# Performance work log

Hardware: AMD Instinct MI355X
Metric: run time of the kernel (lower is better)

Reference implementation:

```python
import jax, jax.numpy as jnp
import numpy as np

B, C = 16, 1024
EPS = 1e-12
TINY = 1e-9


def setup_inputs() -> dict:
    key = jax.random.key(0)
    k1, k2 = jax.random.split(key)
    lower = jax.random.normal(k1, (B, C), dtype=jnp.float32)
    # guarantee upper >= lower as required by bound propagation
    upper = lower + jax.random.uniform(k2, (B, C), dtype=jnp.float32)
    return {"lower": lower, "upper": upper}


def reference(lower, upper):
    l, u = lower, upper
    Bv, Cv = l.shape
    eye = jnp.eye(Cv, dtype=l.dtype)          # (C,C)
    offdiag = 1.0 - eye                        # zero on diagonal

    # pairwise logit differences d_ij = x_j - x_i, bounded by [l_d, u_d]; diag forced to 0
    l_d = (l[:, None, :] - u[:, :, None]) * offdiag   # (B,C,C)
    u_d = (u[:, None, :] - l[:, :, None]) * offdiag   # (B,C,C)

    exp_l = jnp.exp(l_d)
    exp_u = jnp.exp(u_d)

    # exp upper bound: secant over [l_d, u_d]
    denom = u_d - l_d
    a_u = (exp_u - exp_l) / (denom + EPS)
    a_u = jnp.where(jnp.abs(denom) < TINY, exp_u, a_u)
    b_u = exp_l - a_u * l_d

    # exp lower bound: tangent at midpoint t
    t = 0.5 * (l_d + u_d)
    a_l = jnp.exp(t)
    b_l = a_l - a_l * t                        # exp(t) - a_l * t

    # zero diagonal entries (i == j term excluded from the sum)
    a_u = a_u * offdiag
    b_u = b_u * offdiag
    a_l = a_l * offdiag
    b_l = b_l * offdiag
    exp_l_od = exp_l * offdiag
    exp_u_od = exp_u * offdiag

    S_l = exp_l_od.sum(axis=2)                 # (B,C)
    S_u = exp_u_od.sum(axis=2)                 # (B,C)

    # linear coefficients of S_i w.r.t. logits x: off-diag from a, diag collects -sum_j a_ij
    sum_a_u = a_u.sum(axis=2)                  # (B,C)
    sum_a_l = a_l.sum(axis=2)
    coef_S_upper = a_u - eye[None, :, :] * sum_a_u[:, :, None]
    coef_S_lower = a_l - eye[None, :, :] * sum_a_l[:, :, None]
    bias_S_upper = b_u.sum(axis=2)
    bias_S_lower = b_l.sum(axis=2)

    # g(S) = 1 / (1 + S), decreasing & convex
    g_at_S_l = 1.0 / (1.0 + S_l)
    g_at_S_u = 1.0 / (1.0 + S_u)

    # upper relaxation of g: tangent (secant of decreasing convex fn swaps roles)
    denom_g = S_u - S_l
    m_u = (g_at_S_u - g_at_S_l) / (denom_g + EPS)
    m_u = jnp.where(jnp.abs(denom_g) < TINY, -1.0 / (1.0 + S_u) ** 2, m_u)
    c_u = g_at_S_l - m_u * S_l

    # lower relaxation of g: tangent at S_u
    m_l = -1.0 / (1.0 + S_u) ** 2
    c_l = 1.0 / (1.0 + S_u) - m_l * S_u

    # compose (m_u >= ... careful with sign handled as in original: direct product)
    final_upper_coef = m_u[:, :, None] * coef_S_upper   # (B,C,C)
    final_lower_coef = m_l[:, :, None] * coef_S_lower   # (B,C,C)
    final_upper_bias = m_u * bias_S_upper + c_u          # (B,C)
    final_lower_bias = m_l * bias_S_lower + c_l          # (B,C)

    soft_lower = jnp.clip(g_at_S_u, 0.0, 1.0)
    soft_upper = jnp.clip(g_at_S_l, 0.0, 1.0)

    return (soft_lower, soft_upper,
            final_lower_coef, final_upper_coef,
            final_lower_bias, final_upper_bias)
```

## Files before the change

### kernel.cpp

```cpp
#include <hip/hip_runtime.h>

namespace {

constexpr int B = 16;
constexpr int C = 1024;
constexpr int BC = B * C;
constexpr long long BCC = (long long)B * C * C;
constexpr float EPS  = 1e-12f;
constexpr float TINY = 1e-9f;

__global__ __launch_bounds__(256) void bounded_softmax_kernel(
    const float* __restrict__ lower,
    const float* __restrict__ upper,
    float* __restrict__ out)
{
    const int row = blockIdx.x;
    const int b   = row >> 10;
    const int i   = row & (C - 1);
    const int tid = threadIdx.x;

    const float* __restrict__ lrow = lower + b * C;
    const float* __restrict__ urow = upper + b * C;

    const float l_i = lrow[i];
    const float u_i = urow[i];

    const float4 lj4 = *reinterpret_cast<const float4*>(lrow + tid * 4);
    const float4 uj4 = *reinterpret_cast<const float4*>(urow + tid * 4);
    const float ljv[4] = {lj4.x, lj4.y, lj4.z, lj4.w};
    const float ujv[4] = {uj4.x, uj4.y, uj4.z, uj4.w};

    float a_u[4], a_l[4];
    float acc[6] = {0.f, 0.f, 0.f, 0.f, 0.f, 0.f};

    #pragma unroll
    for (int k = 0; k < 4; ++k) {
        const int j = tid * 4 + k;
        const float l_d = ljv[k] - u_i;
        const float u_d = ujv[k] - l_i;
        const float el  = __expf(l_d);
        const float eu  = __expf(u_d);
        const float denom = u_d - l_d;
        float au = (eu - el) / (denom + EPS);
        au = (fabsf(denom) < TINY) ? eu : au;
        const float bu = fmaf(-au, l_d, el);
        const float t  = 0.5f * (l_d + u_d);
        const float al = __expf(t);
        const float bl = al * (1.0f - t);

        float elz = el, euz = eu, auz = au, buz = bu, alz = al, blz = bl;
        if (j == i) { elz = euz = auz = buz = alz = blz = 0.0f; }

        acc[0] += elz; acc[1] += euz; acc[2] += auz;
        acc[3] += alz; acc[4] += buz; acc[5] += blz;
        a_u[k] = auz; a_l[k] = alz;
    }

    __shared__ float red[4][6];
    const int lane = tid & 63;
    const int wid  = tid >> 6;
    #pragma unroll
    for (int m = 0; m < 6; ++m) {
        float v = acc[m];
        #pragma unroll
        for (int o = 32; o > 0; o >>= 1) v += __shfl_down(v, o);
        if (lane == 0) red[wid][m] = v;
    }
    __syncthreads();

    const float S_l  = red[0][0] + red[1][0] + red[2][0] + red[3][0];
    const float S_u  = red[0][1] + red[1][1] + red[2][1] + red[3][1];
    const float SA_u = red[0][2] + red[1][2] + red[2][2] + red[3][2];
    const float SA_l = red[0][3] + red[1][3] + red[2][3] + red[3][3];
    const float SB_u = red[0][4] + red[1][4] + red[2][4] + red[3][4];
    const float SB_l = red[0][5] + red[1][5] + red[2][5] + red[3][5];

    const float g_l = 1.0f / (1.0f + S_l);
    const float g_u = 1.0f / (1.0f + S_u);
    const float dg  = S_u - S_l;
    float m_u = (g_u - g_l) / (dg + EPS);
    m_u = (fabsf(dg) < TINY) ? (-g_u * g_u) : m_u;
    const float c_u = g_l - m_u * S_l;
    const float m_l = -g_u * g_u;
    const float c_l = g_u - m_l * S_u;

    float* __restrict__ lower_coef = out + 2 * BC + (long long)row * C;
    float* __restrict__ upper_coef = out + 2 * BC + BCC + (long long)row * C;

    float lv[4], uv[4];
    #pragma unroll
    for (int k = 0; k < 4; ++k) {
        const int j = tid * 4 + k;
        const float dl = (j == i) ? SA_l : 0.0f;
        const float du = (j == i) ? SA_u : 0.0f;
        lv[k] = m_l * (a_l[k] - dl);
        uv[k] = m_u * (a_u[k] - du);
    }
    *reinterpret_cast<float4*>(lower_coef + tid * 4) =
        make_float4(lv[0], lv[1], lv[2], lv[3]);
    *reinterpret_cast<float4*>(upper_coef + tid * 4) =
        make_float4(uv[0], uv[1], uv[2], uv[3]);

    if (tid == 0) {
        const float soft_lower = fminf(fmaxf(g_u, 0.0f), 1.0f);
        const float soft_upper = fminf(fmaxf(g_l, 0.0f), 1.0f);
        out[row]                          = soft_lower;
        out[BC + row]                     = soft_upper;
        out[2 * BC + 2 * BCC + row]       = fmaf(m_l, SB_l, c_l);
        out[2 * BC + 2 * BCC + BC + row]  = fmaf(m_u, SB_u, c_u);
    }
}

}

extern "C" void kernel_launch(void* const* d_in, const int* in_sizes, int n_in,
                              void* d_out, int out_size, void* d_ws, size_t ws_size,
                              hipStream_t stream) {
    const float* lower = (const float*)d_in[0];
    const float* upper = (const float*)d_in[1];
    float* out = (float*)d_out;
    bounded_softmax_kernel<<<dim3(B * C), dim3(256), 0, stream>>>(lower, upper, out);
}
```

Measured before the change: 149.9 us.

## Factor exponentials into per-element tables and split into three kernels

```diff
diff --git a/kernel.cpp b/kernel.cpp
--- a/kernel.cpp
+++ b/kernel.cpp
@@ -9,105 +9,191 @@
 constexpr float EPS  = 1e-12f;
 constexpr float TINY = 1e-9f;
 
-__global__ __launch_bounds__(256) void bounded_softmax_kernel(
-    const float* __restrict__ lower,
-    const float* __restrict__ upper,
-    float* __restrict__ out)
+typedef float vfloat4 __attribute__((ext_vector_type(4)));
+
+__global__ __launch_bounds__(256) void k0_tables(
+    const float* __restrict__ lower, const float* __restrict__ upper,
+    float* __restrict__ El, float* __restrict__ Eu,
+    float* __restrict__ Em, float* __restrict__ W,
+    float* __restrict__ Bsum)
+{
+    const int b   = blockIdx.x;
+    const int tid = threadIdx.x;
+    const int base = b * C + tid * 4;
+
+    const vfloat4 l4 = *reinterpret_cast<const vfloat4*>(lower + base);
+    const vfloat4 u4 = *reinterpret_cast<const vfloat4*>(upper + base);
+
+    vfloat4 el, eu, em, w;
+    float s0 = 0.f, s1 = 0.f, s2 = 0.f, s3 = 0.f;
+    #pragma unroll
+    for (int k = 0; k < 4; ++k) {
+        const float e_l = __expf(l4[k]);
+        const float e_u = __expf(u4[k]);
+        const float h   = 0.5f * (l4[k] + u4[k]);
+        const float e_m = __expf(h);
+        el[k] = e_l; eu[k] = e_u; em[k] = e_m; w[k] = u4[k] - l4[k];
+        s0 += e_l; s1 += e_u; s2 += e_m; s3 += e_m * (1.0f - h);
+    }
+    *reinterpret_cast<vfloat4*>(El + base) = el;
+    *reinterpret_cast<vfloat4*>(Eu + base) = eu;
+    *reinterpret_cast<vfloat4*>(Em + base) = em;
+    *reinterpret_cast<vfloat4*>(W  + base) = w;
+
+    __shared__ float red[4][4];
+    const int lane = tid & 63, wid = tid >> 6;
+    float v[4] = {s0, s1, s2, s3};
+    #pragma unroll
+    for (int m = 0; m < 4; ++m) {
+        #pragma unroll
+        for (int o = 32; o > 0; o >>= 1) v[m] += __shfl_down(v[m], o);
+        if (lane == 0) red[wid][m] = v[m];
+    }
+    __syncthreads();
+    if (tid == 0) {
+        #pragma unroll
+        for (int m = 0; m < 4; ++m)
+            Bsum[b * 4 + m] = red[0][m] + red[1][m] + red[2][m] + red[3][m];
+    }
+}
+
+__global__ __launch_bounds__(256) void k1_rows(
+    const float* __restrict__ lower, const float* __restrict__ upper,
+    const float* __restrict__ El, const float* __restrict__ Eu,
+    const float* __restrict__ Em, const float* __restrict__ W,
+    const float* __restrict__ Bsum,
+    float* __restrict__ RS, float* __restrict__ out)
 {
     const int row = blockIdx.x;
     const int b   = row >> 10;
-    const int i   = row & (C - 1);
     const int tid = threadIdx.x;
 
-    const float* __restrict__ lrow = lower + b * C;
-    const float* __restrict__ urow = upper + b * C;
-
-    const float l_i = lrow[i];
-    const float u_i = urow[i];
-
-    const float4 lj4 = *reinterpret_cast<const float4*>(lrow + tid * 4);
-    const float4 uj4 = *reinterpret_cast<const float4*>(urow + tid * 4);
-    const float ljv[4] = {lj4.x, lj4.y, lj4.z, lj4.w};
-    const float ujv[4] = {uj4.x, uj4.y, uj4.z, uj4.w};
-
-    float a_u[4], a_l[4];
-    float acc[6] = {0.f, 0.f, 0.f, 0.f, 0.f, 0.f};
-
+    const float l_i  = lower[row], u_i = upper[row];
+    const float El_i = El[row], Eu_i = Eu[row], Em_i = Em[row], w_i = W[row];
+    const float su = __builtin_amdgcn_rcpf(Eu_i);
+    const float sl = __builtin_amdgcn_rcpf(El_i);
+    const float sm = __builtin_amdgcn_rcpf(Em_i);
+
+    const int base = b * C + tid * 4;
+    const vfloat4 El4 = *reinterpret_cast<const vfloat4*>(El + base);
+    const vfloat4 Eu4 = *reinterpret_cast<const vfloat4*>(Eu + base);
+    const vfloat4 W4  = *reinterpret_cast<const vfloat4*>(W  + base);
+    const vfloat4 l4  = *reinterpret_cast<const vfloat4*>(lower + base);
+
+    float accA = 0.f, accT = 0.f;
     #pragma unroll
     for (int k = 0; k < 4; ++k) {
-        const int j = tid * 4 + k;
-        const float l_d = ljv[k] - u_i;
-        const float u_d = ujv[k] - l_i;
-        const float el  = __expf(l_d);
-        const float eu  = __expf(u_d);
-        const float denom = u_d - l_d;
-        float au = (eu - el) / (denom + EPS);
-        au = (fabsf(denom) < TINY) ? eu : au;
-        const float bu = fmaf(-au, l_d, el);
-        const float t  = 0.5f * (l_d + u_d);
-        const float al = __expf(t);
-        const float bl = al * (1.0f - t);
-
-        float elz = el, euz = eu, auz = au, buz = bu, alz = al, blz = bl;
-        if (j == i) { elz = euz = auz = buz = alz = blz = 0.0f; }
-
-        acc[0] += elz; acc[1] += euz; acc[2] += auz;
-        acc[3] += alz; acc[4] += buz; acc[5] += blz;
-        a_u[k] = auz; a_l[k] = alz;
-    }
-
-    __shared__ float red[4][6];
-    const int lane = tid & 63;
-    const int wid  = tid >> 6;
-    #pragma unroll
-    for (int m = 0; m < 6; ++m) {
-        float v = acc[m];
+        const float eu = Eu4[k] * sl;
+        const float el = El4[k] * su;
+        const float denom = W4[k] + w_i;
+        const float r = __builtin_amdgcn_rcpf(denom + EPS);
+        float a = (eu - el) * r;
+        a = (fabsf(denom) < TINY) ? eu : a;
+        accA += a;
+        accT += a * l4[k];
+    }
+
+    __shared__ float red[4][2];
+    const int lane = tid & 63, wid = tid >> 6;
+    #pragma unroll
+    for (int o = 32; o > 0; o >>= 1) accA += __shfl_down(accA, o);
+    #pragma unroll
+    for (int o = 32; o > 0; o >>= 1) accT += __shfl_down(accT, o);
+    if (lane == 0) { red[wid][0] = accA; red[wid][1] = accT; }
+    __syncthreads();
+
+    if (tid == 0) {
+        const float A_all = red[0][0] + red[1][0] + red[2][0] + red[3][0];
+        const float T_all = red[0][1] + red[1][1] + red[2][1] + red[3][1];
+
+        const float eu_d = Eu_i * sl;
+        const float el_d = El_i * su;
+        const float den_d = w_i + w_i;
+        const float r_d = __builtin_amdgcn_rcpf(den_d + EPS);
+        float a_d = (eu_d - el_d) * r_d;
+        a_d = (fabsf(den_d) < TINY) ? eu_d : a_d;
+        const float SA_u = A_all - a_d;
+        const float Tn   = T_all - a_d * l_i;
+
+        const float SEl = Bsum[b * 4 + 0];
+        const float SEu = Bsum[b * 4 + 1];
+        const float P0  = Bsum[b * 4 + 2];
+        const float P1  = Bsum[b * 4 + 3];
+
+        const float S_l  = su * (SEl - El_i);
+        const float S_u  = sl * (SEu - Eu_i);
+        const float SA_l = sm * (P0  - Em_i);
+        const float h_i  = 0.5f * (l_i + u_i);
+        const float SB_l = sm * fmaf(h_i, P0, P1) - 1.0f;
+        const float SB_u = S_l - Tn + u_i * SA_u;
+
+        const float g_l = 1.0f / (1.0f + S_l);
+        const float g_u = 1.0f / (1.0f + S_u);
+        const float dg  = S_u - S_l;
+        float m_u = (g_u - g_l) / (dg + EPS);
+        m_u = (fabsf(dg) < TINY) ? (-g_u * g_u) : m_u;
+        const float c_u = g_l - m_u * S_l;
+        const float m_l = -g_u * g_u;
+        const float c_l = g_u - m_l * S_u;
+
+        out[row]                         = fminf(fmaxf(g_u, 0.0f), 1.0f);
+        out[BC + row]                    = fminf(fmaxf(g_l, 0.0f), 1.0f);
+        out[2 * BC + 2 * BCC + row]      = fmaf(m_l, SB_l, c_l);
+        out[2 * BC + 2 * BCC + BC + row] = fmaf(m_u, SB_u, c_u);
+
+        vfloat4 rs0, rs1;
+        rs0[0] = m_u;  rs0[1] = su;        rs0[2] = sl;         rs0[3] = w_i;
+        rs1[0] = -m_u * SA_u;  rs1[1] = m_l * sm;  rs1[2] = -m_l * SA_l;  rs1[3] = 0.f;
+        *reinterpret_cast<vfloat4*>(RS + (long long)row * 8)     = rs0;
+        *reinterpret_cast<vfloat4*>(RS + (long long)row * 8 + 4) = rs1;
+    }
+}
+
+__global__ __launch_bounds__(256) void k2_stream(
+    const float* __restrict__ El, const float* __restrict__ Eu,
+    const float* __restrict__ Em, const float* __restrict__ W,
+    const float* __restrict__ RS, float* __restrict__ out)
+{
+    const int blk = blockIdx.x;
+    const int b   = blk >> 8;
+    const int ig  = blk & 255;
+    const int tid = threadIdx.x;
+    const int j0  = tid * 4;
+    const int tbase = b * C + j0;
+
+    const vfloat4 El4 = *reinterpret_cast<const vfloat4*>(El + tbase);
+    const vfloat4 Eu4 = *reinterpret_cast<const vfloat4*>(Eu + tbase);
+    const vfloat4 Em4 = *reinterpret_cast<const vfloat4*>(Em + tbase);
+    const vfloat4 W4  = *reinterpret_cast<const vfloat4*>(W  + tbase);
+
+    float* __restrict__ lower_base = out + 2 * BC;
+    float* __restrict__ upper_base = out + 2 * BC + BCC;
+
+    #pragma unroll
+    for (int r = 0; r < 4; ++r) {
+        const int i   = ig * 4 + r;
+        const int row = b * C + i;
+        const vfloat4 rs0 = *reinterpret_cast<const vfloat4*>(RS + (long long)row * 8);
+        const vfloat4 rs1 = *reinterpret_cast<const vfloat4*>(RS + (long long)row * 8 + 4);
+        const float m_u = rs0[0], su = rs0[1], sl = rs0[2], w_i = rs0[3];
+        const float DiagU = rs1[0], MlE = rs1[1], DiagL = rs1[2];
+
+        vfloat4 up, lo;
         #pragma unroll
-        for (int o = 32; o > 0; o >>= 1) v += __shfl_down(v, o);
-        if (lane == 0) red[wid][m] = v;
-    }
-    __syncthreads();
-
-    const float S_l  = red[0][0] + red[1][0] + red[2][0] + red[3][0];
-    const float S_u  = red[0][1] + red[1][1] + red[2][1] + red[3][1];
-    const float SA_u = red[0][2] + red[1][2] + red[2][2] + red[3][2];
-    const float SA_l = red[0][3] + red[1][3] + red[2][3] + red[3][3];
-    const float SB_u = red[0][4] + red[1][4] + red[2][4] + red[3][4];
-    const float SB_l = red[0][5] + red[1][5] + red[2][5] + red[3][5];
-
-    const float g_l = 1.0f / (1.0f + S_l);
-    const float g_u = 1.0f / (1.0f + S_u);
-    const float dg  = S_u - S_l;
-    float m_u = (g_u - g_l) / (dg + EPS);
-    m_u = (fabsf(dg) < TINY) ? (-g_u * g_u) : m_u;
-    const float c_u = g_l - m_u * S_l;
-    const float m_l = -g_u * g_u;
-    const float c_l = g_u - m_l * S_u;
-
-    float* __restrict__ lower_coef = out + 2 * BC + (long long)row * C;
-    float* __restrict__ upper_coef = out + 2 * BC + BCC + (long long)row * C;
-
-    float lv[4], uv[4];
-    #pragma unroll
-    for (int k = 0; k < 4; ++k) {
-        const int j = tid * 4 + k;
-        const float dl = (j == i) ? SA_l : 0.0f;
-        const float du = (j == i) ? SA_u : 0.0f;
-        lv[k] = m_l * (a_l[k] - dl);
-        uv[k] = m_u * (a_u[k] - du);
-    }
-    *reinterpret_cast<float4*>(lower_coef + tid * 4) =
-        make_float4(lv[0], lv[1], lv[2], lv[3]);
-    *reinterpret_cast<float4*>(upper_coef + tid * 4) =
-        make_float4(uv[0], uv[1], uv[2], uv[3]);
-
-    if (tid == 0) {
-        const float soft_lower = fminf(fmaxf(g_u, 0.0f), 1.0f);
-        const float soft_upper = fminf(fmaxf(g_l, 0.0f), 1.0f);
-        out[row]                          = soft_lower;
-        out[BC + row]                     = soft_upper;
-        out[2 * BC + 2 * BCC + row]       = fmaf(m_l, SB_l, c_l);
-        out[2 * BC + 2 * BCC + BC + row]  = fmaf(m_u, SB_u, c_u);
+        for (int k = 0; k < 4; ++k) {
+            const float eu = Eu4[k] * sl;
+            const float el = El4[k] * su;
+            const float denom = W4[k] + w_i;
+            const float rc = __builtin_amdgcn_rcpf(denom + EPS);
+            float a = (eu - el) * rc;
+            a = (fabsf(denom) < TINY) ? eu : a;
+            up[k] = m_u * a;
+            lo[k] = MlE * Em4[k];
+            if (j0 + k == i) { up[k] = DiagU; lo[k] = DiagL; }
+        }
+        const long long off = (long long)row * C + j0;
+        __builtin_nontemporal_store(lo, reinterpret_cast<vfloat4*>(lower_base + off));
+        __builtin_nontemporal_store(up, reinterpret_cast<vfloat4*>(upper_base + off));
     }
 }
 
@@ -119,5 +205,15 @@
     const float* lower = (const float*)d_in[0];
     const float* upper = (const float*)d_in[1];
     float* out = (float*)d_out;
-    bounded_softmax_kernel<<<dim3(B * C), dim3(256), 0, stream>>>(lower, upper, out);
-}
+
+    float* El   = (float*)d_ws;
+    float* Eu   = El + BC;
+    float* Em   = Eu + BC;
+    float* W    = Em + BC;
+    float* Bsum = W + BC;
+    float* RS   = Bsum + 64;
+
+    k0_tables<<<dim3(B), dim3(256), 0, stream>>>(lower, upper, El, Eu, Em, W, Bsum);
+    k1_rows<<<dim3(BC), dim3(256), 0, stream>>>(lower, upper, El, Eu, Em, W, Bsum, RS, out);
+    k2_stream<<<dim3(4096), dim3(256), 0, stream>>>(El, Eu, Em, W, RS, out);
+}
```

Result: slower. 159.9 us (+6.7%).
